# Kernel optimization log

Measured on AMD Instinct MI355X. Metric: run time of the kernel, lower is better.

Reference implementation:

```python
import jax, jax.numpy as jnp
import numpy as np
import math

KV_STRIDE = 2
Q_STRIDE = 1
WAVE_LEN = 1000.0
POS_MAG = 1.0


def _pos_embed(h, w, h_kv, w_kv, q_stride, kv_stride, feat_dim):
    # Sinusoidal relative-position embeddings, matching get_position_embedding.
    h_idx = jnp.arange(h, dtype=jnp.float32) * q_stride
    w_idx = jnp.arange(w, dtype=jnp.float32) * q_stride
    h_kv_idx = jnp.arange(h_kv, dtype=jnp.float32) * kv_stride
    w_kv_idx = jnp.arange(w_kv, dtype=jnp.float32) * kv_stride
    h_diff = (h_idx[:, None] - h_kv_idx[None, :]) * POS_MAG  # (h, h_kv)
    w_diff = (w_idx[:, None] - w_kv_idx[None, :]) * POS_MAG  # (w, w_kv)
    feat_range = jnp.arange(feat_dim // 4, dtype=jnp.float32)
    dim_mat = WAVE_LEN ** (4.0 / feat_dim * feat_range)  # (feat_dim//4,)
    wd = w_diff[:, :, None] / dim_mat  # (w, w_kv, F)
    hd = h_diff[:, :, None] / dim_mat  # (h, h_kv, F)
    emb_x = jnp.concatenate([jnp.sin(wd), jnp.cos(wd)], axis=2)  # (w, w_kv, feat_dim//2)
    emb_y = jnp.concatenate([jnp.sin(hd), jnp.cos(hd)], axis=2)  # (h, h_kv, feat_dim//2)
    return emb_x, emb_y


def setup_inputs() -> dict:
    key = jax.random.key(0)
    ks = jax.random.split(key, 11)
    C = 288
    s = 1.0 / math.sqrt(C)
    return {
        'x_input': jax.random.normal(ks[0], (2, C, 64, 64), jnp.float32),
        'Wq': jax.random.normal(ks[1], (C, C), jnp.float32) * s,
        'Wk': jax.random.normal(ks[2], (C, C), jnp.float32) * s,
        'Wv': jax.random.normal(ks[3], (C, C), jnp.float32) * s,
        'Wx': jax.random.normal(ks[4], (C, C // 2), jnp.float32) * s,
        'Wy': jax.random.normal(ks[5], (C, C // 2), jnp.float32) * s,
        'Wproj': jax.random.normal(ks[6], (C, C), jnp.float32) * s,
        'bproj': jax.random.normal(ks[7], (C,), jnp.float32) * 0.02,
        'Wc': jax.random.normal(ks[8], (9, C), jnp.float32) * s,
        'bc': jax.random.normal(ks[9], (9,), jnp.float32) * 0.02,
        'gamma': jax.random.normal(ks[10], (1,), jnp.float32),
    }


def reference(x_input, Wq, Wk, Wv, Wx, Wy, Wproj, bproj, Wc, bc, gamma):
    M = Wc.shape[0]                       # num_mixtures
    n, C, h, w = x_input.shape
    d = Wq.shape[0] // M                  # qk_embed_dim (== v_dim)
    x_q = x_input                         # q_stride == 1
    x_kv = x_input[:, :, ::KV_STRIDE, ::KV_STRIDE]  # AvgPool2d(k=1, stride=2)
    h_kv, w_kv = x_kv.shape[2], x_kv.shape[3]

    # 1x1 convs as channel GEMMs
    q = jnp.einsum('nchw,oc->nohw', x_q, Wq).reshape(n, M, d, h * w)
    q = q.transpose(0, 1, 3, 2)                                    # (n,M,hw,d)
    k = jnp.einsum('nchw,oc->nohw', x_kv, Wk).reshape(n, M, d, h_kv * w_kv)

    emb_x, emb_y = _pos_embed(h, w, h_kv, w_kv, Q_STRIDE, KV_STRIDE, C)
    inv_sqrt2 = 1.0 / math.sqrt(2.0)
    pf_x = (emb_x @ Wx.T).reshape(w, w_kv, M, d).transpose(2, 0, 1, 3) * inv_sqrt2  # (M,w,w_kv,d)
    pf_y = (emb_y @ Wy.T).reshape(h, h_kv, M, d).transpose(2, 0, 1, 3) * inv_sqrt2  # (M,h,h_kv,d)

    energy = jnp.matmul(q, k).reshape(n, M, h, w, h_kv, w_kv)
    q5 = q.reshape(n, M, h, w, d)
    e_x = jnp.einsum('nmhwd,mwvd->nmhwv', q5, pf_x)  # (n,M,h,w,w_kv)
    e_y = jnp.einsum('nmhwd,mhud->nmhwu', q5, pf_y)  # (n,M,h,w,h_kv)
    energy = energy + e_x[:, :, :, :, None, :] + e_y[:, :, :, :, :, None]
    energy = energy.reshape(n, M, h * w, h_kv * w_kv)
    attn = jax.nn.softmax(energy, axis=3)

    # Learned per-mixture gating from mean query context
    context = q.transpose(0, 1, 3, 2).reshape(n, M * d, h * w).mean(axis=2)  # (n, M*d)
    mix_w = jax.nn.softmax(context @ Wc.T + bc, axis=1)                      # (n, M)
    attn = jnp.sum(attn * mix_w[:, :, None, None], axis=1)                   # (n,hw,hw_kv)

    v = jnp.einsum('nchw,oc->nohw', x_kv, Wv).reshape(n, M * d, h_kv * w_kv)
    v = v.transpose(0, 2, 1)                                                 # (n,hw_kv,M*d)
    out = jnp.matmul(attn, v).transpose(0, 2, 1).reshape(n, M * d, h, w)
    out = jnp.einsum('nchw,oc->nohw', out, Wproj) + bproj[None, :, None, None]
    return gamma[0] * out + x_input
```

## Files before the change

### kernel.cpp

```cpp
#include <hip/hip_runtime.h>
#include <math.h>

#define NB     2
#define CDIM   288
#define HW     4096
#define PKV    1024
#define MHEAD  9
#define DHEAD  32

typedef __attribute__((ext_vector_type(8))) short bf16x8;
typedef __attribute__((ext_vector_type(4))) float f32x4;

__device__ inline unsigned short f2bf(float x) {
    unsigned int u = __float_as_uint(x);
    u = (u + 0x7fffu + ((u >> 16) & 1u)) >> 16;
    return (unsigned short)u;
}


__global__ __launch_bounds__(256) void prep(const float* __restrict__ X,
        const float* __restrict__ Wq, const float* __restrict__ Wk,
        const float* __restrict__ Wv, const float* __restrict__ Wproj,
        const float* __restrict__ Wx, const float* __restrict__ Wy,
        unsigned short* __restrict__ XF, unsigned short* __restrict__ WFq,
        unsigned short* __restrict__ WFk, unsigned short* __restrict__ WFv,
        unsigned short* __restrict__ WFp, float* __restrict__ WTx,
        float* __restrict__ WTy, float* __restrict__ MX) {
    __shared__ float t32[32][133];
    __shared__ float t16[16][17];
    __shared__ float red[4];
    int b = blockIdx.x;
    int tid = threadIdx.x;
    if (b < 576) {
        int bx = b % 32, by = (b / 32) % 9, n = b / 288;
        int j0 = bx * 128, c0 = by * 32;
        int c = tid >> 3, f = tid & 7;
        const float* src = &X[((size_t)n * CDIM + c0 + c) * HW + j0];
#pragma unroll
        for (int l = 0; l < 4; ++l) {
            float4 v = *(const float4*)&src[(f + l * 8) * 4];
            *(float4*)&t32[c][(f + l * 8) * 4] = v;
        }
        __syncthreads();
        int cc = c0 >> 5;
#pragma unroll
        for (int l = 0; l < 4; ++l) {
            int g = l * 256 + tid;
            int s = g >> 7;
            int w = g & 127;
            int lane = w >> 1, e0 = (w & 1) * 4;
            int jl = s * 16 + (lane & 15);
            int cb = (lane >> 4) * 8 + e0;
            unsigned int w0 = f2bf(t32[cb + 0][jl]) | ((unsigned int)f2bf(t32[cb + 1][jl]) << 16);
            unsigned int w1 = f2bf(t32[cb + 2][jl]) | ((unsigned int)f2bf(t32[cb + 3][jl]) << 16);
            int jt = (j0 >> 4) + s;
            unsigned short* O = XF + (size_t)n * HW * CDIM + ((size_t)jt * 9 + cc) * 512 + lane * 8 + e0;
            uint2 pk = { w0, w1 };
            *(uint2*)O = pk;
        }
    } else if (b < 900) {
        int u = b - 576;
        int bx = u % 9, by = (u / 9) % 18, bz = u / 162;
        const float* W = bz ? Wy : Wx;
        float* WT      = bz ? WTy : WTx;
        int f0 = bx * 16, o0 = by * 16;
        int tx = tid & 15, ty = tid >> 4;
        t16[ty][tx] = W[(o0 + ty) * 144 + f0 + tx];
        __syncthreads();
        WT[(f0 + ty) * 288 + o0 + tx] = t16[tx][ty];
    } else if (b < 1062) {
        int t = b - 900;
        int sub = tid >> 6, lane = tid & 63;
        int ot = t / 9, cc = t % 9;
        const float* W = (sub == 0) ? Wq : (sub == 1) ? Wk : (sub == 2) ? Wv : Wproj;
        unsigned short* O = ((sub == 0) ? WFq : (sub == 1) ? WFk : (sub == 2) ? WFv : WFp)
                            + (size_t)t * 512;
        int o  = ot * 16 + (lane & 15);
        int c0 = cc * 32 + (lane >> 4) * 8;
        const float* src = W + (size_t)o * CDIM + c0;
        float4 f0 = *(const float4*)src, f1 = *(const float4*)(src + 4);
        unsigned int v0 = f2bf(f0.x) | ((unsigned int)f2bf(f0.y) << 16);
        unsigned int v1 = f2bf(f0.z) | ((unsigned int)f2bf(f0.w) << 16);
        unsigned int v2 = f2bf(f1.x) | ((unsigned int)f2bf(f1.y) << 16);
        unsigned int v3 = f2bf(f1.z) | ((unsigned int)f2bf(f1.w) << 16);
        uint4 pk = { v0, v1, v2, v3 };
        *(uint4*)(O + lane * 8) = pk;
    } else {
        int bid = b - 1062;
        const float* xr = X + (size_t)bid * HW;
        float s = 0.f;
        for (int j = tid; j < HW; j += 256) s += xr[j];
        for (int off = 32; off > 0; off >>= 1) s += __shfl_xor(s, off, 64);
        if ((tid & 63) == 0) red[tid >> 6] = s;
        __syncthreads();
        if (tid == 0) MX[bid] = (red[0] + red[1] + red[2] + red[3]) * (1.f / 4096.f);
    }
}

__global__ __launch_bounds__(256) void mid(
        const float* __restrict__ WTx, const float* __restrict__ WTy,
        unsigned short* __restrict__ FXb, unsigned short* __restrict__ FYb,
        const float* __restrict__ Wq, const float* __restrict__ MX,
        const float* __restrict__ Wc, const float* __restrict__ bc,
        float* __restrict__ MIXW,
        const unsigned short* __restrict__ WFq, const unsigned short* __restrict__ WFk,
        const unsigned short* __restrict__ WFv, const unsigned short* __restrict__ XF,
        unsigned short* __restrict__ Qf, unsigned short* __restrict__ KF,
        unsigned short* __restrict__ VF) {
    __shared__ float emb[144];
    __shared__ float ctx_s[NB * CDIM];
    __shared__ float lg[18];
    __shared__ __attribute__((aligned(16))) unsigned short tr[4][32][40];
    int b = blockIdx.x;
    int tid = threadIdx.x;

    if (b < 252) {
        int axis = b / 126;
        int dif  = b % 126;
        float diff = (float)(dif - 62);
        if (tid < 72) {
            float dm = expf(6.9077552789821368f * ((float)tid * (1.f / 72.f)));
            float t  = diff / dm;
            emb[tid]      = sinf(t);
            emb[72 + tid] = cosf(t);
        }
        __syncthreads();
        const float* WT = axis ? WTy : WTx;
        unsigned short* F = axis ? FYb : FXb;
        for (int o = tid; o < CDIM; o += 256) {
            float s = 0.f;
#pragma unroll 8
            for (int f = 0; f < 144; ++f) s += emb[f] * WT[f * 288 + o];
            int m = o >> 5, d = o & 31;
            F[(size_t)(m * 8 + (dif >> 4)) * 512 + ((dif & 15) + 16 * (d >> 3)) * 8 + (d & 7)]
                = f2bf(s * 0.70710678118654752f);
        }
    } else if (b == 252) {
        for (int idx = tid; idx < 1152; idx += 256) {
            int d = idx & 31, rr = (idx >> 5) & 1, mm = (idx >> 6) % 9, ax = idx / 576;
            int dif = 126 + rr;
            unsigned short* F = ax ? FYb : FXb;
            F[(size_t)(mm * 8 + 7) * 512 + ((dif & 15) + 16 * (d >> 3)) * 8 + (d & 7)] = 0;
        }
        for (int p = tid; p < NB * CDIM; p += 256) {
            int n = p / CDIM, o = p % CDIM;
            const float* wr = Wq + (size_t)o * CDIM;
            const float* mx = MX + n * CDIM;
            float s = 0.f;
            for (int c = 0; c < CDIM; c += 4) {
                float4 w4 = *(const float4*)&wr[c];
                float4 m4 = *(const float4*)&mx[c];
                s += w4.x * m4.x + w4.y * m4.y + w4.z * m4.z + w4.w * m4.w;
            }
            ctx_s[p] = s;
        }
        __syncthreads();
        if (tid < 18) {
            int n = tid / 9, j = tid % 9;
            float s = bc[j];
            for (int o = 0; o < CDIM; ++o) s += ctx_s[n * CDIM + o] * Wc[j * CDIM + o];
            lg[tid] = s;
        }
        __syncthreads();
        if (tid < 2) {
            float mx = -1e30f;
            for (int j = 0; j < 9; ++j) mx = fmaxf(mx, lg[tid * 9 + j]);
            float e[9], sm = 0.f;
            for (int j = 0; j < 9; ++j) { e[j] = __expf(lg[tid * 9 + j] - mx); sm += e[j]; }
            for (int j = 0; j < 9; ++j) MIXW[tid * 9 + j] = e[j] / sm;
        }
    } else {
        int bx = b - 253;
        int gx = bx % 40;
        int m  = (bx / 40) % 9;
        int n  = bx / 360;
        int wv = tid >> 6, lane = tid & 63;
        int lq = lane & 15, quad = lane >> 4;
        if (gx < 32) {
            int j0 = gx * 128;
            int jw = j0 + wv * 32;
            const unsigned short* Wb = WFq + ((size_t)(m * 2) * 9) * 512 + lane * 8;
            const unsigned short* Xb = XF + (size_t)n * HW * CDIM + ((size_t)(jw >> 4) * 9) * 512 + lane * 8;
            f32x4 acc[2][2] = {};
#pragma unroll
            for (int cc = 0; cc < 9; ++cc) {
                bf16x8 a0 = *(const bf16x8*)(Wb + (size_t)cc * 512);
                bf16x8 a1 = *(const bf16x8*)(Wb + (size_t)(9 + cc) * 512);
                bf16x8 b0 = *(const bf16x8*)(Xb + (size_t)cc * 512);
                bf16x8 b1 = *(const bf16x8*)(Xb + (size_t)(9 + cc) * 512);
                acc[0][0] = __builtin_amdgcn_mfma_f32_16x16x32_bf16(a0, b0, acc[0][0], 0, 0, 0);
                acc[0][1] = __builtin_amdgcn_mfma_f32_16x16x32_bf16(a0, b1, acc[0][1], 0, 0, 0);
                acc[1][0] = __builtin_amdgcn_mfma_f32_16x16x32_bf16(a1, b0, acc[1][0], 0, 0, 0);
                acc[1][1] = __builtin_amdgcn_mfma_f32_16x16x32_bf16(a1, b1, acc[1][1], 0, 0, 0);
            }
#pragma unroll
            for (int oi = 0; oi < 2; ++oi)
#pragma unroll
                for (int ji = 0; ji < 2; ++ji)
#pragma unroll
                    for (int r = 0; r < 4; ++r)
                        tr[wv][ji * 16 + lq][oi * 16 + quad * 4 + r] = f2bf(acc[oi][ji][r]);
            int jl = lane & 31, half = lane >> 5;
            bf16x8 v0 = *(const bf16x8*)&tr[wv][jl][half * 16];
            bf16x8 v1 = *(const bf16x8*)&tr[wv][jl][half * 16 + 8];
            unsigned short* Qm = Qf + ((size_t)(n * MHEAD + m) * HW + jw + jl) * 32 + half * 16;
            *(bf16x8*)Qm = v0;
            *(bf16x8*)(Qm + 8) = v1;
        } else {
            int p0 = (gx - 32) * 128;
            int pw = p0 + wv * 32;
            const unsigned short* XFn = XF + (size_t)n * HW * CDIM;
            size_t bidx[2];
#pragma unroll
            for (int pi = 0; pi < 2; ++pi) {
                int p   = pw + pi * 16 + lq;
                int pos = ((p >> 5) << 7) + ((p & 31) << 1);
                bidx[pi] = ((size_t)(pos >> 4) * 9) * 512 + ((pos & 15) + 16 * quad) * 8;
            }
            const unsigned short* Wkb = WFk + ((size_t)(m * 2) * 9) * 512 + lane * 8;
            const unsigned short* Wvb = WFv + ((size_t)(m * 2) * 9) * 512 + lane * 8;
            f32x4 ak[2][2] = {}, av[2][2] = {};
#pragma unroll
            for (int cc = 0; cc < 9; ++cc) {
                bf16x8 a0k = *(const bf16x8*)(Wkb + (size_t)cc * 512);
                bf16x8 a1k = *(const bf16x8*)(Wkb + (size_t)(9 + cc) * 512);
                bf16x8 a0v = *(const bf16x8*)(Wvb + (size_t)cc * 512);
                bf16x8 a1v = *(const bf16x8*)(Wvb + (size_t)(9 + cc) * 512);
                bf16x8 b0  = *(const bf16x8*)(XFn + bidx[0] + (size_t)cc * 512);
                bf16x8 b1  = *(const bf16x8*)(XFn + bidx[1] + (size_t)cc * 512);
                ak[0][0] = __builtin_amdgcn_mfma_f32_16x16x32_bf16(a0k, b0, ak[0][0], 0, 0, 0);
                ak[0][1] = __builtin_amdgcn_mfma_f32_16x16x32_bf16(a0k, b1, ak[0][1], 0, 0, 0);
                ak[1][0] = __builtin_amdgcn_mfma_f32_16x16x32_bf16(a1k, b0, ak[1][0], 0, 0, 0);
                ak[1][1] = __builtin_amdgcn_mfma_f32_16x16x32_bf16(a1k, b1, ak[1][1], 0, 0, 0);
                av[0][0] = __builtin_amdgcn_mfma_f32_16x16x32_bf16(a0v, b0, av[0][0], 0, 0, 0);
                av[0][1] = __builtin_amdgcn_mfma_f32_16x16x32_bf16(a0v, b1, av[0][1], 0, 0, 0);
                av[1][0] = __builtin_amdgcn_mfma_f32_16x16x32_bf16(a1v, b0, av[1][0], 0, 0, 0);
                av[1][1] = __builtin_amdgcn_mfma_f32_16x16x32_bf16(a1v, b1, av[1][1], 0, 0, 0);
            }
#pragma unroll
            for (int oi = 0; oi < 2; ++oi)
#pragma unroll
                for (int pi = 0; pi < 2; ++pi)
#pragma unroll
                    for (int r = 0; r < 4; ++r)
                        tr[wv][pi * 16 + lq][oi * 16 + quad * 4 + r] = f2bf(ak[oi][pi][r]);
            unsigned short* KFm = KF + (size_t)(n * MHEAD + m) * (PKV * 32);
#pragma unroll
            for (int pi = 0; pi < 2; ++pi) {
                bf16x8 v = *(const bf16x8*)&tr[wv][pi * 16 + lq][quad * 8];
                *(bf16x8*)(KFm + (size_t)((pw >> 4) + pi) * 512 + lane * 8) = v;
            }
#pragma unroll
            for (int oi = 0; oi < 2; ++oi)
#pragma unroll
                for (int pi = 0; pi < 2; ++pi)
#pragma unroll
                    for (int r = 0; r < 4; ++r)
                        tr[wv][oi * 16 + quad * 4 + r][pi * 16 + lq] = f2bf(av[oi][pi][r]);
            unsigned short* VFn = VF + (size_t)n * CDIM * PKV;
#pragma unroll
            for (int oi = 0; oi < 2; ++oi) {
                bf16x8 v = *(const bf16x8*)&tr[wv][oi * 16 + lq][quad * 8];
                *(bf16x8*)(VFn + (size_t)((m * 2 + oi) * 32 + (pw >> 5)) * 512 + lane * 8) = v;
            }
        }
    }
}

__global__ __launch_bounds__(512, 4) void attn_fused4(
        const unsigned short* __restrict__ Qf, const unsigned short* __restrict__ KF,
        const unsigned short* __restrict__ VF, const unsigned short* __restrict__ WFp,
        const unsigned short* __restrict__ FXb, const unsigned short* __restrict__ FYb,
        const float* __restrict__ MIXW, const float* __restrict__ bproj,
        const float* __restrict__ x, const float* __restrict__ gamma,
        float* __restrict__ OUT) {
    int n    = blockIdx.x >> 8;
    int i0   = (blockIdx.x & 255) * 16;
    int tid  = threadIdx.x;
    int wv   = tid >> 6;
    int lane = tid & 63;
    int lq   = lane & 15;
    int quad = lane >> 4;

    int bx_t = (i0 & 63) >> 4;
    int h    = i0 >> 6;
    int by_t = h >> 4;
    int dh   = h & 15;

    __shared__ __attribute__((aligned(16))) unsigned char RM[10752];
    float (*Rx_s)[82] = (float (*)[82])RM;
    float (*Ry_s)[82] = (float (*)[82])(RM + 5248);
    unsigned short (*Mt)[296] = (unsigned short (*)[296])RM;
    __shared__ __attribute__((aligned(16))) float ws_s[16][8];
    __shared__ __attribute__((aligned(16))) unsigned short tr[16][1032];

    float mixed[8][4];
#pragma unroll
    for (int t = 0; t < 8; ++t)
#pragma unroll
        for (int j = 0; j < 4; ++j) mixed[t][j] = 0.f;

    for (int m = 0; m < MHEAD; ++m) {
        const unsigned short* Qm  = Qf + ((size_t)(n * MHEAD + m) * HW + i0) * 32;
        const unsigned short* KmF = KF + (size_t)(n * MHEAD + m) * (PKV * 32);
        bf16x8 afrag = *(const bf16x8*)(Qm + (size_t)lq * 32 + quad * 8);

        if (wv < 5) {
            bf16x8 bR = *(const bf16x8*)(FXb + (size_t)(m * 8 + bx_t + wv) * 512 + lane * 8);
            f32x4 r = (f32x4){0.f, 0.f, 0.f, 0.f};
            r = __builtin_amdgcn_mfma_f32_16x16x32_bf16(afrag, bR, r, 0, 0, 0);
#pragma unroll
            for (int reg = 0; reg < 4; ++reg)
                Rx_s[quad * 4 + reg][wv * 16 + lq] = r[reg];
        } else {
            bf16x8 bR = *(const bf16x8*)(FYb + (size_t)(m * 8 + by_t + (wv - 5)) * 512 + lane * 8);
            f32x4 r = (f32x4){0.f, 0.f, 0.f, 0.f};
            r = __builtin_amdgcn_mfma_f32_16x16x32_bf16(afrag, bR, r, 0, 0, 0);
#pragma unroll
            for (int reg = 0; reg < 4; ++reg)
                Ry_s[quad * 4 + reg][(wv - 5) * 16 + lq] = r[reg];
        }
        if (wv < 2) {
            bf16x8 bR = *(const bf16x8*)(FYb + (size_t)(m * 8 + by_t + 3 + wv) * 512 + lane * 8);
            f32x4 r = (f32x4){0.f, 0.f, 0.f, 0.f};
            r = __builtin_amdgcn_mfma_f32_16x16x32_bf16(afrag, bR, r, 0, 0, 0);
#pragma unroll
            for (int reg = 0; reg < 4; ++reg)
                Ry_s[quad * 4 + reg][(3 + wv) * 16 + lq] = r[reg];
        }
        __syncthreads();

        bf16x8 kf[8];
#pragma unroll
        for (int t = 0; t < 8; ++t)
            kf[t] = *(const bf16x8*)(KmF + (size_t)(wv * 8 + t) * 512 + lane * 8);
        f32x4 acc[8];
#pragma unroll
        for (int t = 0; t < 8; ++t) acc[t] = (f32x4){0.f, 0.f, 0.f, 0.f};
#pragma unroll
        for (int t = 0; t < 8; ++t)
            acc[t] = __builtin_amdgcn_mfma_f32_16x16x32_bf16(afrag, kf[t], acc[t], 0, 0, 0);

        float exA[4], exB[4];
#pragma unroll
        for (int j = 0; j < 4; ++j) {
            int q = quad * 4 + j;
            exA[j] = Rx_s[q][q + 62 - 2 * lq];
            exB[j] = Rx_s[q][q + 30 - 2 * lq];
        }

        float rs[4] = {0.f, 0.f, 0.f, 0.f};
#pragma unroll
        for (int tp = 0; tp < 4; ++tp) {
            int u = wv * 4 + tp;
            float ey[4];
#pragma unroll
            for (int j = 0; j < 4; ++j) ey[j] = Ry_s[quad * 4 + j][dh + 62 - 2 * u];
#pragma unroll
            for (int half = 0; half < 2; ++half) {
                int t = tp * 2 + half;
#pragma unroll
                for (int j = 0; j < 4; ++j) {
                    float e = __expf(acc[t][j] + (half ? exB[j] : exA[j]) + ey[j]);
                    rs[j] += e;
                    acc[t][j] = e;
                }
            }
        }
#pragma unroll
        for (int j = 0; j < 4; ++j) {
            rs[j] += __shfl_xor(rs[j], 1, 64);
            rs[j] += __shfl_xor(rs[j], 2, 64);
            rs[j] += __shfl_xor(rs[j], 4, 64);
            rs[j] += __shfl_xor(rs[j], 8, 64);
        }
        if (lq == 0) {
#pragma unroll
            for (int j = 0; j < 4; ++j) ws_s[quad * 4 + j][wv] = rs[j];
        }
        __syncthreads();

        float wm = MIXW[n * MHEAD + m];
#pragma unroll
        for (int j = 0; j < 4; ++j) {
            int q = quad * 4 + j;
            float4 w0 = *(const float4*)&ws_s[q][0];
            float4 w1 = *(const float4*)&ws_s[q][4];
            float lt = (w0.x + w0.y) + (w0.z + w0.w) + (w1.x + w1.y) + (w1.z + w1.w);
            float fct = wm / lt;
#pragma unroll
            for (int t = 0; t < 8; ++t) mixed[t][j] += acc[t][j] * fct;
        }
    }

#pragma unroll
    for (int t = 0; t < 8; ++t)
#pragma unroll
        for (int j = 0; j < 4; ++j)
            tr[quad * 4 + j][wv * 128 + t * 16 + lq] = f2bf(mixed[t][j]);
    __syncthreads();

    const unsigned short* VFn = VF + (size_t)n * CDIM * PKV;
    f32x4 accpv[3];
#pragma unroll
    for (int idx = 0; idx < 3; ++idx) accpv[idx] = (f32x4){0.f, 0.f, 0.f, 0.f};
#pragma unroll 4
    for (int pc = 0; pc < 32; ++pc) {
        bf16x8 pf = *(const bf16x8*)&tr[lq][pc * 32 + quad * 8];
#pragma unroll
        for (int idx = 0; idx < 3; ++idx) {
            int ot = wv + idx * 8;
            if (ot < 18) {
                bf16x8 vf = *(const bf16x8*)(VFn + (size_t)(ot * 32 + pc) * 512 + lane * 8);
                accpv[idx] = __builtin_amdgcn_mfma_f32_16x16x32_bf16(pf, vf, accpv[idx], 0, 0, 0);
            }
        }
    }
#pragma unroll
    for (int idx = 0; idx < 3; ++idx) {
        int ot = wv + idx * 8;
        if (ot < 18) {
#pragma unroll
            for (int r = 0; r < 4; ++r)
                Mt[quad * 4 + r][ot * 16 + lq] = f2bf(accpv[idx][r]);
        }
    }
    __syncthreads();

    float g = gamma[0];
#pragma unroll
    for (int idx = 0; idx < 3; ++idx) {
        int ot = wv + idx * 8;
        if (ot >= 18) continue;
        f32x4 acc = (f32x4){0.f, 0.f, 0.f, 0.f};
#pragma unroll
        for (int cc = 0; cc < 9; ++cc) {
            bf16x8 af = *(const bf16x8*)(WFp + (size_t)(ot * 9 + cc) * 512 + lane * 8);
            bf16x8 bfm = *(const bf16x8*)&Mt[lq][cc * 32 + quad * 8];
            acc = __builtin_amdgcn_mfma_f32_16x16x32_bf16(af, bfm, acc, 0, 0, 0);
        }
#pragma unroll
        for (int r = 0; r < 4; ++r) {
            int o = ot * 16 + quad * 4 + r;
            size_t id = ((size_t)(n * CDIM) + o) * HW + i0 + lq;
            OUT[id] = g * (acc[r] + bproj[o]) + x[id];
        }
    }
}

extern "C" void kernel_launch(void* const* d_in, const int* in_sizes, int n_in,
                              void* d_out, int out_size, void* d_ws, size_t ws_size,
                              hipStream_t stream) {
    const float* x     = (const float*)d_in[0];
    const float* Wq    = (const float*)d_in[1];
    const float* Wk    = (const float*)d_in[2];
    const float* Wv    = (const float*)d_in[3];
    const float* Wx    = (const float*)d_in[4];
    const float* Wy    = (const float*)d_in[5];
    const float* Wproj = (const float*)d_in[6];
    const float* bproj = (const float*)d_in[7];
    const float* Wc    = (const float*)d_in[8];
    const float* bc    = (const float*)d_in[9];
    const float* gamma = (const float*)d_in[10];
    float* out = (float*)d_out;

    float* ws = (float*)d_ws;
    size_t off = 0;
    unsigned short* Qf  = (unsigned short*)(ws + off); off += (size_t)NB * MHEAD * HW * 32 / 2;
    unsigned short* KF  = (unsigned short*)(ws + off); off += (size_t)NB * MHEAD * PKV * 32 / 2;
    unsigned short* VF  = (unsigned short*)(ws + off); off += (size_t)NB * CDIM * PKV / 2;
    unsigned short* WFq = (unsigned short*)(ws + off); off += (size_t)CDIM * CDIM / 2;
    unsigned short* WFk = (unsigned short*)(ws + off); off += (size_t)CDIM * CDIM / 2;
    unsigned short* WFv = (unsigned short*)(ws + off); off += (size_t)CDIM * CDIM / 2;
    unsigned short* WFp = (unsigned short*)(ws + off); off += (size_t)CDIM * CDIM / 2;
    unsigned short* XF  = (unsigned short*)(ws + off); off += (size_t)NB * HW * CDIM / 2;
    float* WTx  = ws + off; off += 144 * 288;
    float* WTy  = ws + off; off += 144 * 288;
    unsigned short* FXb = (unsigned short*)(ws + off); off += (size_t)MHEAD * 8 * 512 / 2;
    unsigned short* FYb = (unsigned short*)(ws + off); off += (size_t)MHEAD * 8 * 512 / 2;
    float* MX   = ws + off; off += NB * CDIM;
    float* MIXW = ws + off; off += 32;

    prep<<<1638, 256, 0, stream>>>(x, Wq, Wk, Wv, Wproj, Wx, Wy,
                                   XF, WFq, WFk, WFv, WFp, WTx, WTy, MX);
    mid<<<973, 256, 0, stream>>>(WTx, WTy, FXb, FYb, Wq, MX, Wc, bc, MIXW,
                                 WFq, WFk, WFv, XF, Qf, KF, VF);
    attn_fused4<<<NB * HW / 16, 512, 0, stream>>>(Qf, KF, VF, WFp, FXb, FYb, MIXW,
                                                  bproj, x, gamma, out);
}
```

Baseline: 179.2 us.

## Software-pipeline attention head loop with double-buffered LDS and exp2

Restructures the per-head loop in the fused attention kernel so that the relative-position MFMAs for head m+1 and the deferred normalisation and mixing of head m-1 overlap with the QK MFMAs of head m. Rx/Ry/ws shared buffers are double-buffered, which drops one __syncthreads per head. Q is prescaled by log2(e) in the mid kernel so the softmax can use the hardware exp2 instruction, and s_setprio raises wave priority around the MFMA section. This costs more LDS and more live registers, which may affect occupancy at 512 threads with 4 blocks per CU.

```diff
diff --git a/kernel.cpp b/kernel.cpp
--- a/kernel.cpp
+++ b/kernel.cpp
@@ -10,6 +10,12 @@
 
 typedef __attribute__((ext_vector_type(8))) short bf16x8;
 typedef __attribute__((ext_vector_type(4))) float f32x4;
+
+#if __has_builtin(__builtin_amdgcn_exp2f)
+#define EXP2(x) __builtin_amdgcn_exp2f(x)
+#else
+#define EXP2(x) exp2f(x)
+#endif
 
 __device__ inline unsigned short f2bf(float x) {
     unsigned int u = __float_as_uint(x);
@@ -199,7 +205,8 @@
                 for (int ji = 0; ji < 2; ++ji)
 #pragma unroll
                     for (int r = 0; r < 4; ++r)
-                        tr[wv][ji * 16 + lq][oi * 16 + quad * 4 + r] = f2bf(acc[oi][ji][r]);
+                        tr[wv][ji * 16 + lq][oi * 16 + quad * 4 + r]
+                            = f2bf(1.4426950408889634f * acc[oi][ji][r]);
             int jl = lane & 31, half = lane >> 5;
             bf16x8 v0 = *(const bf16x8*)&tr[wv][jl][half * 16];
             bf16x8 v1 = *(const bf16x8*)&tr[wv][jl][half * 16 + 8];
@@ -267,7 +274,7 @@
     }
 }
 
-__global__ __launch_bounds__(512, 4) void attn_fused4(
+__global__ __launch_bounds__(512, 4) void attn_fused5(
         const unsigned short* __restrict__ Qf, const unsigned short* __restrict__ KF,
         const unsigned short* __restrict__ VF, const unsigned short* __restrict__ WFp,
         const unsigned short* __restrict__ FXb, const unsigned short* __restrict__ FYb,
@@ -287,81 +294,106 @@
     int by_t = h >> 4;
     int dh   = h & 15;
 
-    __shared__ __attribute__((aligned(16))) unsigned char RM[10752];
-    float (*Rx_s)[82] = (float (*)[82])RM;
-    float (*Ry_s)[82] = (float (*)[82])(RM + 5248);
-    unsigned short (*Mt)[296] = (unsigned short (*)[296])RM;
-    __shared__ __attribute__((aligned(16))) float ws_s[16][8];
+    __shared__ __attribute__((aligned(16))) float Rx_s[2][16][82];
+    __shared__ __attribute__((aligned(16))) float Ry_s[2][16][82];
+    __shared__ __attribute__((aligned(16))) float ws_s[2][16][8];
     __shared__ __attribute__((aligned(16))) unsigned short tr[16][1032];
+    unsigned short (*Mt)[296] = (unsigned short (*)[296])&Rx_s[0][0][0];
 
     float mixed[8][4];
 #pragma unroll
     for (int t = 0; t < 8; ++t)
 #pragma unroll
         for (int j = 0; j < 4; ++j) mixed[t][j] = 0.f;
+    f32x4 acc[8];
+
+    auto r_phase = [&](int mm, bf16x8 af) {
+        int pp = mm & 1;
+        if (wv < 5) {
+            bf16x8 bR = *(const bf16x8*)(FXb + (size_t)(mm * 8 + bx_t + wv) * 512 + lane * 8);
+            f32x4 r = (f32x4){0.f, 0.f, 0.f, 0.f};
+            r = __builtin_amdgcn_mfma_f32_16x16x32_bf16(af, bR, r, 0, 0, 0);
+#pragma unroll
+            for (int reg = 0; reg < 4; ++reg)
+                Rx_s[pp][quad * 4 + reg][wv * 16 + lq] = r[reg];
+        } else {
+            bf16x8 bR = *(const bf16x8*)(FYb + (size_t)(mm * 8 + by_t + (wv - 5)) * 512 + lane * 8);
+            f32x4 r = (f32x4){0.f, 0.f, 0.f, 0.f};
+            r = __builtin_amdgcn_mfma_f32_16x16x32_bf16(af, bR, r, 0, 0, 0);
+#pragma unroll
+            for (int reg = 0; reg < 4; ++reg)
+                Ry_s[pp][quad * 4 + reg][(wv - 5) * 16 + lq] = r[reg];
+        }
+        if (wv < 2) {
+            bf16x8 bR = *(const bf16x8*)(FYb + (size_t)(mm * 8 + by_t + 3 + wv) * 512 + lane * 8);
+            f32x4 r = (f32x4){0.f, 0.f, 0.f, 0.f};
+            r = __builtin_amdgcn_mfma_f32_16x16x32_bf16(af, bR, r, 0, 0, 0);
+#pragma unroll
+            for (int reg = 0; reg < 4; ++reg)
+                Ry_s[pp][quad * 4 + reg][(3 + wv) * 16 + lq] = r[reg];
+        }
+    };
+
+    bf16x8 af_cur = *(const bf16x8*)(Qf + (((size_t)n * MHEAD) * HW + i0 + lq) * 32 + quad * 8);
+    r_phase(0, af_cur);
+    __syncthreads();
 
     for (int m = 0; m < MHEAD; ++m) {
-        const unsigned short* Qm  = Qf + ((size_t)(n * MHEAD + m) * HW + i0) * 32;
         const unsigned short* KmF = KF + (size_t)(n * MHEAD + m) * (PKV * 32);
-        bf16x8 afrag = *(const bf16x8*)(Qm + (size_t)lq * 32 + quad * 8);
-
-        if (wv < 5) {
-            bf16x8 bR = *(const bf16x8*)(FXb + (size_t)(m * 8 + bx_t + wv) * 512 + lane * 8);
-            f32x4 r = (f32x4){0.f, 0.f, 0.f, 0.f};
-            r = __builtin_amdgcn_mfma_f32_16x16x32_bf16(afrag, bR, r, 0, 0, 0);
-#pragma unroll
-            for (int reg = 0; reg < 4; ++reg)
-                Rx_s[quad * 4 + reg][wv * 16 + lq] = r[reg];
-        } else {
-            bf16x8 bR = *(const bf16x8*)(FYb + (size_t)(m * 8 + by_t + (wv - 5)) * 512 + lane * 8);
-            f32x4 r = (f32x4){0.f, 0.f, 0.f, 0.f};
-            r = __builtin_amdgcn_mfma_f32_16x16x32_bf16(afrag, bR, r, 0, 0, 0);
-#pragma unroll
-            for (int reg = 0; reg < 4; ++reg)
-                Ry_s[quad * 4 + reg][(wv - 5) * 16 + lq] = r[reg];
-        }
-        if (wv < 2) {
-            bf16x8 bR = *(const bf16x8*)(FYb + (size_t)(m * 8 + by_t + 3 + wv) * 512 + lane * 8);
-            f32x4 r = (f32x4){0.f, 0.f, 0.f, 0.f};
-            r = __builtin_amdgcn_mfma_f32_16x16x32_bf16(afrag, bR, r, 0, 0, 0);
-#pragma unroll
-            for (int reg = 0; reg < 4; ++reg)
-                Ry_s[quad * 4 + reg][(3 + wv) * 16 + lq] = r[reg];
-        }
-        __syncthreads();
-
         bf16x8 kf[8];
 #pragma unroll
         for (int t = 0; t < 8; ++t)
             kf[t] = *(const bf16x8*)(KmF + (size_t)(wv * 8 + t) * 512 + lane * 8);
-        f32x4 acc[8];
-#pragma unroll
-        for (int t = 0; t < 8; ++t) acc[t] = (f32x4){0.f, 0.f, 0.f, 0.f};
-#pragma unroll
-        for (int t = 0; t < 8; ++t)
-            acc[t] = __builtin_amdgcn_mfma_f32_16x16x32_bf16(afrag, kf[t], acc[t], 0, 0, 0);
-
+
+        if (m) {
+            int pr = (m - 1) & 1;
+            float wm = MIXW[n * MHEAD + m - 1];
+#pragma unroll
+            for (int j = 0; j < 4; ++j) {
+                int q = quad * 4 + j;
+                float4 w0 = *(const float4*)&ws_s[pr][q][0];
+                float4 w1 = *(const float4*)&ws_s[pr][q][4];
+                float lt = (w0.x + w0.y) + (w0.z + w0.w) + (w1.x + w1.y) + (w1.z + w1.w);
+                float fct = wm / lt;
+#pragma unroll
+                for (int t = 0; t < 8; ++t) mixed[t][j] += acc[t][j] * fct;
+            }
+        }
+
+        bf16x8 af_nxt = af_cur;
+        __builtin_amdgcn_s_setprio(1);
+        if (m + 1 < MHEAD) {
+            af_nxt = *(const bf16x8*)(Qf + (((size_t)(n * MHEAD + m + 1)) * HW + i0 + lq) * 32 + quad * 8);
+            r_phase(m + 1, af_nxt);
+        }
+#pragma unroll
+        for (int t = 0; t < 8; ++t) {
+            f32x4 z = (f32x4){0.f, 0.f, 0.f, 0.f};
+            acc[t] = __builtin_amdgcn_mfma_f32_16x16x32_bf16(af_cur, kf[t], z, 0, 0, 0);
+        }
+        __builtin_amdgcn_s_setprio(0);
+
+        int par = m & 1;
         float exA[4], exB[4];
 #pragma unroll
         for (int j = 0; j < 4; ++j) {
             int q = quad * 4 + j;
-            exA[j] = Rx_s[q][q + 62 - 2 * lq];
-            exB[j] = Rx_s[q][q + 30 - 2 * lq];
-        }
-
+            exA[j] = Rx_s[par][q][q + 62 - 2 * lq];
+            exB[j] = Rx_s[par][q][q + 30 - 2 * lq];
+        }
         float rs[4] = {0.f, 0.f, 0.f, 0.f};
 #pragma unroll
         for (int tp = 0; tp < 4; ++tp) {
             int u = wv * 4 + tp;
             float ey[4];
 #pragma unroll
-            for (int j = 0; j < 4; ++j) ey[j] = Ry_s[quad * 4 + j][dh + 62 - 2 * u];
+            for (int j = 0; j < 4; ++j) ey[j] = Ry_s[par][quad * 4 + j][dh + 62 - 2 * u];
 #pragma unroll
             for (int half = 0; half < 2; ++half) {
                 int t = tp * 2 + half;
 #pragma unroll
                 for (int j = 0; j < 4; ++j) {
-                    float e = __expf(acc[t][j] + (half ? exB[j] : exA[j]) + ey[j]);
+                    float e = EXP2(acc[t][j] + (half ? exB[j] : exA[j]) + ey[j]);
                     rs[j] += e;
                     acc[t][j] = e;
                 }
@@ -376,16 +408,19 @@
         }
         if (lq == 0) {
 #pragma unroll
-            for (int j = 0; j < 4; ++j) ws_s[quad * 4 + j][wv] = rs[j];
-        }
-        __syncthreads();
-
-        float wm = MIXW[n * MHEAD + m];
+            for (int j = 0; j < 4; ++j) ws_s[par][quad * 4 + j][wv] = rs[j];
+        }
+        __syncthreads();
+        af_cur = af_nxt;
+    }
+
+    {
+        float wm = MIXW[n * MHEAD + 8];
 #pragma unroll
         for (int j = 0; j < 4; ++j) {
             int q = quad * 4 + j;
-            float4 w0 = *(const float4*)&ws_s[q][0];
-            float4 w1 = *(const float4*)&ws_s[q][4];
+            float4 w0 = *(const float4*)&ws_s[0][q][0];
+            float4 w1 = *(const float4*)&ws_s[0][q][4];
             float lt = (w0.x + w0.y) + (w0.z + w0.w) + (w1.x + w1.y) + (w1.z + w1.w);
             float fct = wm / lt;
 #pragma unroll
@@ -432,18 +467,18 @@
     for (int idx = 0; idx < 3; ++idx) {
         int ot = wv + idx * 8;
         if (ot >= 18) continue;
-        f32x4 acc = (f32x4){0.f, 0.f, 0.f, 0.f};
+        f32x4 acco = (f32x4){0.f, 0.f, 0.f, 0.f};
 #pragma unroll
         for (int cc = 0; cc < 9; ++cc) {
             bf16x8 af = *(const bf16x8*)(WFp + (size_t)(ot * 9 + cc) * 512 + lane * 8);
             bf16x8 bfm = *(const bf16x8*)&Mt[lq][cc * 32 + quad * 8];
-            acc = __builtin_amdgcn_mfma_f32_16x16x32_bf16(af, bfm, acc, 0, 0, 0);
+            acco = __builtin_amdgcn_mfma_f32_16x16x32_bf16(af, bfm, acco, 0, 0, 0);
         }
 #pragma unroll
         for (int r = 0; r < 4; ++r) {
             int o = ot * 16 + quad * 4 + r;
             size_t id = ((size_t)(n * CDIM) + o) * HW + i0 + lq;
-            OUT[id] = g * (acc[r] + bproj[o]) + x[id];
+            OUT[id] = g * (acco[r] + bproj[o]) + x[id];
         }
     }
 }
@@ -485,6 +520,6 @@
                                    XF, WFq, WFk, WFv, WFp, WTx, WTy, MX);
     mid<<<973, 256, 0, stream>>>(WTx, WTy, FXb, FYb, Wq, MX, Wc, bc, MIXW,
                                  WFq, WFk, WFv, XF, Qf, KF, VF);
-    attn_fused4<<<NB * HW / 16, 512, 0, stream>>>(Qf, KF, VF, WFp, FXb, FYb, MIXW,
+    attn_fused5<<<NB * HW / 16, 512, 0, stream>>>(Qf, KF, VF, WFp, FXb, FYb, MIXW,
                                                   bproj, x, gamma, out);
 }
```

After: 281.4 us. 57.0% more time.
